# Optimization experiments

Measured on AMD Instinct MI355X. Metric: run time of the kernel, lower is better.

Reference implementation:

```python
import jax, jax.numpy as jnp
import numpy as np

ALPHA = 1.0
EPS = 1e-8

def setup_inputs() -> dict:
    key = jax.random.key(0)
    k1, k2, k3 = jax.random.split(key, 3)
    B, L, S, H, E, D = 4, 2048, 2048, 8, 64, 64
    queries = jax.random.normal(k1, (B, L, H, E), dtype=jnp.float32)
    keys = jax.random.normal(k2, (B, S, H, E), dtype=jnp.float32)
    values = jax.random.normal(k3, (B, S, H, D), dtype=jnp.float32)
    return {"queries": queries, "keys": keys, "values": values}

def reference(queries, keys, values):
    E = queries.shape[3]
    scale = 1.0 / jnp.sqrt(jnp.asarray(E, queries.dtype))
    # dot_product: [B,H,L,S]
    dot = jnp.einsum('blhe,bshe->bhls', queries, keys)
    q_norm2 = jnp.sum(queries ** 2, axis=-1).transpose(0, 2, 1)[..., :, None]  # [B,H,L,1]
    k_norm2 = jnp.sum(keys ** 2, axis=-1).transpose(0, 2, 1)[..., None, :]     # [B,H,1,S]
    wedge2 = jax.nn.relu(q_norm2 * k_norm2 - dot ** 2)
    wedge = jnp.sqrt(wedge2 + EPS)
    scores = ((1.0 - ALPHA) * dot + ALPHA * wedge) * scale
    A = jax.nn.softmax(scores, axis=-1)  # dropout in eval mode = identity
    out = jnp.einsum('bhls,bshd->blhd', A, values)
    return out
```

## Files before the change

### kernel.cpp

```cpp
#include <hip/hip_runtime.h>

typedef __attribute__((ext_vector_type(4))) float f32x4;
typedef __attribute__((ext_vector_type(4))) float float4v;
typedef __attribute__((ext_vector_type(8))) short bf16x8;
typedef __attribute__((ext_vector_type(8))) unsigned short ushort8;

#define DEVI static __device__ __forceinline__

namespace {
constexpr int kL = 2048, kS = 2048, kH = 8;
constexpr int QB = 64, KVB = 64, NKT = kS / KVB;
constexpr float kC = 0.18033688f;
constexpr float kEpsC = 3.252139e-10f;
constexpr int KTILE = 8448;
constexpr int VTILE = 8192;
constexpr int KBH = 32 * KTILE;
constexpr int VBH = 32 * VTILE;
}

DEVI int swz(int byteoff) { return byteoff ^ (((byteoff >> 7) & 7) << 4); }

DEVI unsigned cvtpk(float lo, float hi) {
  unsigned r;
  asm("v_cvt_pk_bf16_f32 %0, %1, %2" : "=v"(r) : "v"(lo), "v"(hi));
  return r;
}

__global__ __launch_bounds__(256) void prep_k(const float* __restrict__ Kg,
                                              char* __restrict__ Kb) {
  const int chunk = (int)blockIdx.x * 256 + (int)threadIdx.x;
  const int tile = chunk >> 9;
  const int i = chunk & 511;
  const int bh = tile >> 5, kt = tile & 31;
  const int b = bh >> 3, h = bh & 7;
  const int row = i >> 3;
  const int colsel = (i & 7) ^ (row & 7);
  const int s = kt * 64 + row;
  const float* src = Kg + (((size_t)b * kS + s) * kH + h) * 64 + colsel * 8;
  float4v v0 = *(const float4v*)(src);
  float4v v1 = *(const float4v*)(src + 4);
  float pn = v0.x*v0.x + v0.y*v0.y + v0.z*v0.z + v0.w*v0.w
           + v1.x*v1.x + v1.y*v1.y + v1.z*v1.z + v1.w*v1.w;
  union { unsigned w[4]; ushort8 u; } o;
  o.w[0] = cvtpk(v0.x, v0.y); o.w[1] = cvtpk(v0.z, v0.w);
  o.w[2] = cvtpk(v1.x, v1.y); o.w[3] = cvtpk(v1.z, v1.w);
  char* tb = Kb + (size_t)tile * KTILE;
  *(ushort8*)(tb + i * 16) = o.u;
  pn += __shfl_xor(pn, 1);
  pn += __shfl_xor(pn, 2);
  pn += __shfl_xor(pn, 4);
  if ((i & 7) == 0) *(float*)(tb + 8192 + row * 4) = pn;
}

__global__ __launch_bounds__(256) void prep_v(const float* __restrict__ Vg,
                                              char* __restrict__ Vt) {
  __shared__ char tile[64 * 128];
  const int t = (int)threadIdx.x;
  const int bid = (int)blockIdx.x;
  const int st = bid & 31, bh = bid >> 5;
  const int b = bh >> 3, h = bh & 7;
  {
    const int sl = t >> 2, c0 = (t & 3) * 16;
    const float* src = Vg + (((size_t)b * kS + st * 64 + sl) * kH + h) * 64 + c0;
    float4v v0 = *(const float4v*)(src);
    float4v v1 = *(const float4v*)(src + 4);
    float4v v2 = *(const float4v*)(src + 8);
    float4v v3 = *(const float4v*)(src + 12);
    union { unsigned w[4]; ushort8 u; } t0, t1;
    t0.w[0] = cvtpk(v0.x, v0.y); t0.w[1] = cvtpk(v0.z, v0.w);
    t0.w[2] = cvtpk(v1.x, v1.y); t0.w[3] = cvtpk(v1.z, v1.w);
    t1.w[0] = cvtpk(v2.x, v2.y); t1.w[1] = cvtpk(v2.z, v2.w);
    t1.w[2] = cvtpk(v3.x, v3.y); t1.w[3] = cvtpk(v3.z, v3.w);
    *(ushort8*)(tile + swz(sl * 128 + c0 * 2)) = t0.u;
    *(ushort8*)(tile + swz(sl * 128 + c0 * 2 + 16)) = t1.u;
  }
  __syncthreads();
  char* dst = Vt + (size_t)bid * VTILE;
#pragma unroll
  for (int cc = 0; cc < 2; ++cc) {
    const int i = t * 2 + cc;
    const int z = swz(i * 16);
    const int d = z >> 7;
    const int k0 = ((z >> 4) & 7) * 8;
    union { unsigned short s[8]; ushort8 u; } o;
#pragma unroll
    for (int j = 0; j < 8; ++j) {
      const int k = k0 + j;
      const int sig = (((k >> 5) * 2 + ((k & 7) >> 2)) << 4) |
                      (((k >> 3) & 3) << 2) | (k & 3);
      o.s[j] = *(const unsigned short*)(tile + swz(sig * 128 + d * 2));
    }
    *(ushort8*)(dst + i * 16) = o.u;
  }
}

__global__ __launch_bounds__(256) void geo_attn_kernel(
    const float* __restrict__ Qg, const char* __restrict__ Kb,
    const char* __restrict__ Vt, float* __restrict__ Og) {
  __shared__ char lds[2][16384];

  const int t = (int)threadIdx.x;
  const int wv = t >> 6, lane = t & 63, gg = lane >> 4, cl = lane & 15;
  const int bh = (int)blockIdx.y, b = bh >> 3, h = bh & 7;
  const int l0 = (int)blockIdx.x * QB;

  const int q = l0 + wv * 16 + cl;
  const float* qp = Qg + (((size_t)b * kL + q) * kH + h) * 64;
  float4v x0 = *(const float4v*)(qp + gg * 8);
  float4v x1 = *(const float4v*)(qp + gg * 8 + 4);
  float4v x2 = *(const float4v*)(qp + gg * 8 + 32);
  float4v x3 = *(const float4v*)(qp + gg * 8 + 36);
  x0 *= kC; x1 *= kC; x2 *= kC; x3 *= kC;
  float pn = 0.f;
#pragma unroll
  for (int j = 0; j < 4; ++j) {
    pn = fmaf(x0[j], x0[j], pn); pn = fmaf(x1[j], x1[j], pn);
    pn = fmaf(x2[j], x2[j], pn); pn = fmaf(x3[j], x3[j], pn);
  }
  union frag { bf16x8 v; unsigned w[4]; };
  frag qb0, qb1;
  qb0.w[0] = cvtpk(x0.x, x0.y); qb0.w[1] = cvtpk(x0.z, x0.w);
  qb0.w[2] = cvtpk(x1.x, x1.y); qb0.w[3] = cvtpk(x1.z, x1.w);
  qb1.w[0] = cvtpk(x2.x, x2.y); qb1.w[1] = cvtpk(x2.z, x2.w);
  qb1.w[2] = cvtpk(x3.x, x3.y); qb1.w[3] = cvtpk(x3.z, x3.w);
  pn += __shfl_xor(pn, 16);
  pn += __shfl_xor(pn, 32);
  const float qn2 = pn;

  const char* gsrc0 = (wv < 2) ? (Kb + (size_t)bh * KBH) : (Vt + (size_t)bh * VBH);
  const int gstride = (wv < 2) ? KTILE : VTILE;
  const char* gp = gsrc0 + (wv & 1) * 4096 + lane * 16;
  const char* ktail = Kb + (size_t)bh * KBH + 8192;

#define STAGE(BUF) do { \
    char* _lb = lds[BUF] + wv * 4096; \
    __builtin_amdgcn_global_load_lds((__attribute__((address_space(1))) void*)(gp),        (__attribute__((address_space(3))) void*)(_lb),        16, 0, 0); \
    __builtin_amdgcn_global_load_lds((__attribute__((address_space(1))) void*)(gp + 1024), (__attribute__((address_space(3))) void*)(_lb + 1024), 16, 0, 0); \
    __builtin_amdgcn_global_load_lds((__attribute__((address_space(1))) void*)(gp + 2048), (__attribute__((address_space(3))) void*)(_lb + 2048), 16, 0, 0); \
    __builtin_amdgcn_global_load_lds((__attribute__((address_space(1))) void*)(gp + 3072), (__attribute__((address_space(3))) void*)(_lb + 3072), 16, 0, 0); \
  } while (0)

  float lsum = 0.f;
  f32x4 oacc[4];
#pragma unroll
  for (int dt = 0; dt < 4; ++dt) oacc[dt] = (f32x4){0.f, 0.f, 0.f, 0.f};

  STAGE(0);
  gp += gstride;
  __syncthreads();

  int cur = 0;
  for (int kt = 0; kt < NKT; ++kt) {
    if (kt + 1 < NKT) { STAGE(cur ^ 1); gp += gstride; }

    float4v kn2v[4];
#pragma unroll
    for (int nt = 0; nt < 4; ++nt)
      kn2v[nt] = *(const float4v*)(ktail + nt * 64 + gg * 16);
    ktail += KTILE;

    const char* ksc = lds[cur];
    const char* vsc = lds[cur] + 8192;

    f32x4 dacc[4];
#pragma unroll
    for (int nt = 0; nt < 4; ++nt) {
      bf16x8 ka0 = *(const bf16x8*)(ksc + swz((nt * 16 + cl) * 128 + gg * 16));
      bf16x8 ka1 = *(const bf16x8*)(ksc + swz((nt * 16 + cl) * 128 + gg * 16 + 64));
      f32x4 acc = {0.f, 0.f, 0.f, 0.f};
      acc = __builtin_amdgcn_mfma_f32_16x16x32_bf16(ka0, qb0.v, acc, 0, 0, 0);
      acc = __builtin_amdgcn_mfma_f32_16x16x32_bf16(ka1, qb1.v, acc, 0, 0, 0);
      dacc[nt] = acc;
    }

    float sc[4][4];
#pragma unroll
    for (int nt = 0; nt < 4; ++nt)
#pragma unroll
      for (int r = 0; r < 4; ++r) {
        const float dot = dacc[nt][r];
        float w2 = fmaf(-dot, dot, qn2 * kn2v[nt][r]);
        w2 = fmaxf(w2, kEpsC);
        const float p = __builtin_amdgcn_exp2f(__builtin_amdgcn_sqrtf(w2));
        sc[nt][r] = p;
        lsum += p;
      }

    frag pa0, pa1;
    pa0.w[0] = cvtpk(sc[0][0], sc[0][1]); pa0.w[1] = cvtpk(sc[0][2], sc[0][3]);
    pa0.w[2] = cvtpk(sc[1][0], sc[1][1]); pa0.w[3] = cvtpk(sc[1][2], sc[1][3]);
    pa1.w[0] = cvtpk(sc[2][0], sc[2][1]); pa1.w[1] = cvtpk(sc[2][2], sc[2][3]);
    pa1.w[2] = cvtpk(sc[3][0], sc[3][1]); pa1.w[3] = cvtpk(sc[3][2], sc[3][3]);

#pragma unroll
    for (int dt = 0; dt < 4; ++dt) {
      bf16x8 vb0 = *(const bf16x8*)(vsc + swz((dt * 16 + cl) * 128 + gg * 16));
      bf16x8 vb1 = *(const bf16x8*)(vsc + swz((dt * 16 + cl) * 128 + gg * 16 + 64));
      f32x4 acc = oacc[dt];
      acc = __builtin_amdgcn_mfma_f32_16x16x32_bf16(pa0.v, vb0, acc, 0, 0, 0);
      acc = __builtin_amdgcn_mfma_f32_16x16x32_bf16(pa1.v, vb1, acc, 0, 0, 0);
      oacc[dt] = acc;
    }

    __syncthreads();
    cur ^= 1;
  }
#undef STAGE

  lsum += __shfl_xor(lsum, 16);
  lsum += __shfl_xor(lsum, 32);
  const float inv = 1.f / lsum;
  float inv4[4];
#pragma unroll
  for (int r = 0; r < 4; ++r)
    inv4[r] = __shfl(inv, (lane & 48) | (gg * 4 + r));
#pragma unroll
  for (int r = 0; r < 4; ++r) {
    const int l = l0 + wv * 16 + gg * 4 + r;
    float* op = Og + (((size_t)b * kL + l) * kH + h) * 64;
#pragma unroll
    for (int dt = 0; dt < 4; ++dt)
      op[dt * 16 + cl] = oacc[dt][r] * inv4[r];
  }
}

extern "C" void kernel_launch(void* const* d_in, const int* in_sizes, int n_in,
                              void* d_out, int out_size, void* d_ws, size_t ws_size,
                              hipStream_t stream) {
  const float* Qg = (const float*)d_in[0];
  const float* Kg = (const float*)d_in[1];
  const float* Vg = (const float*)d_in[2];
  float* Og = (float*)d_out;
  char* Kb = (char*)d_ws;
  char* Vt = (char*)d_ws + (size_t)1024 * KTILE;
  prep_k<<<2048, 256, 0, stream>>>(Kg, Kb);
  prep_v<<<1024, 256, 0, stream>>>(Vg, Vt);
  dim3 grid(kL / QB, 32);
  geo_attn_kernel<<<grid, dim3(256), 0, stream>>>(Qg, Kb, Vt, Og);
}
```

Measured before the change: 83.96 us.

## Software-pipeline PV MFMA one tile behind QK with triple-buffered V

Restructures the KV loop so the P·V MFMAs for the previous tile run right after the current tile's Q·K MFMAs, before the transcendental score math. The aim is to overlap matrix-core work with the sqrt/exp2 VALU work. K stays double-buffered while V gets a third LDS buffer so the previous tile's V remains valid. This raises LDS use from 32KB to 40KB per block, which may lower occupancy, and adds an epilogue that drains the last pending PV step.

Result: no change. 84.57 us (+0.7%).

```diff
diff --git a/kernel.cpp b/kernel.cpp
--- a/kernel.cpp
+++ b/kernel.cpp
@@ -97,7 +97,8 @@
 __global__ __launch_bounds__(256) void geo_attn_kernel(
     const float* __restrict__ Qg, const char* __restrict__ Kb,
     const char* __restrict__ Vt, float* __restrict__ Og) {
-  __shared__ char lds[2][16384];
+  __shared__ char kbuf[2][8192];
+  __shared__ char vbuf[3][8192];
 
   const int t = (int)threadIdx.x;
   const int wv = t >> 6, lane = t & 63, gg = lane >> 4, cl = lane & 15;
@@ -127,13 +128,14 @@
   pn += __shfl_xor(pn, 32);
   const float qn2 = pn;
 
-  const char* gsrc0 = (wv < 2) ? (Kb + (size_t)bh * KBH) : (Vt + (size_t)bh * VBH);
-  const int gstride = (wv < 2) ? KTILE : VTILE;
-  const char* gp = gsrc0 + (wv & 1) * 4096 + lane * 16;
+  const bool isK = (wv < 2);
+  const char* gp = (isK ? Kb + (size_t)bh * KBH : Vt + (size_t)bh * VBH)
+                   + (wv & 1) * 4096 + lane * 16;
+  const int gstride = isK ? KTILE : VTILE;
   const char* ktail = Kb + (size_t)bh * KBH + 8192;
 
-#define STAGE(BUF) do { \
-    char* _lb = lds[BUF] + wv * 4096; \
+#define STAGE(DSTBASE) do { \
+    char* _lb = (DSTBASE) + (wv & 1) * 4096; \
     __builtin_amdgcn_global_load_lds((__attribute__((address_space(1))) void*)(gp),        (__attribute__((address_space(3))) void*)(_lb),        16, 0, 0); \
     __builtin_amdgcn_global_load_lds((__attribute__((address_space(1))) void*)(gp + 1024), (__attribute__((address_space(3))) void*)(_lb + 1024), 16, 0, 0); \
     __builtin_amdgcn_global_load_lds((__attribute__((address_space(1))) void*)(gp + 2048), (__attribute__((address_space(3))) void*)(_lb + 2048), 16, 0, 0); \
@@ -145,67 +147,89 @@
 #pragma unroll
   for (int dt = 0; dt < 4; ++dt) oacc[dt] = (f32x4){0.f, 0.f, 0.f, 0.f};
 
-  STAGE(0);
+  STAGE(isK ? kbuf[0] : vbuf[0]);
   gp += gstride;
   __syncthreads();
 
-  int cur = 0;
+  char* kr = kbuf[0]; char* kst = kbuf[1];
+  char* vr = vbuf[2]; char* vm = vbuf[0]; char* vst = vbuf[1];
+  frag pa0, pa1;
+  pa0.w[0] = pa0.w[1] = pa0.w[2] = pa0.w[3] = 0u;
+  pa1.w[0] = pa1.w[1] = pa1.w[2] = pa1.w[3] = 0u;
+
   for (int kt = 0; kt < NKT; ++kt) {
-    if (kt + 1 < NKT) { STAGE(cur ^ 1); gp += gstride; }
+    if (kt + 1 < NKT) {
+      STAGE(isK ? kst : vst);
+      gp += gstride;
+    }
 
     float4v kn2v[4];
 #pragma unroll
     for (int nt = 0; nt < 4; ++nt)
       kn2v[nt] = *(const float4v*)(ktail + nt * 64 + gg * 16);
     ktail += KTILE;
-
-    const char* ksc = lds[cur];
-    const char* vsc = lds[cur] + 8192;
+    float qk2[4][4];
+#pragma unroll
+    for (int nt = 0; nt < 4; ++nt)
+#pragma unroll
+      for (int r = 0; r < 4; ++r) qk2[nt][r] = qn2 * kn2v[nt][r];
 
     f32x4 dacc[4];
 #pragma unroll
     for (int nt = 0; nt < 4; ++nt) {
-      bf16x8 ka0 = *(const bf16x8*)(ksc + swz((nt * 16 + cl) * 128 + gg * 16));
-      bf16x8 ka1 = *(const bf16x8*)(ksc + swz((nt * 16 + cl) * 128 + gg * 16 + 64));
+      bf16x8 ka0 = *(const bf16x8*)(kr + swz((nt * 16 + cl) * 128 + gg * 16));
+      bf16x8 ka1 = *(const bf16x8*)(kr + swz((nt * 16 + cl) * 128 + gg * 16 + 64));
       f32x4 acc = {0.f, 0.f, 0.f, 0.f};
       acc = __builtin_amdgcn_mfma_f32_16x16x32_bf16(ka0, qb0.v, acc, 0, 0, 0);
       acc = __builtin_amdgcn_mfma_f32_16x16x32_bf16(ka1, qb1.v, acc, 0, 0, 0);
       dacc[nt] = acc;
     }
 
+    if (kt > 0) {
+#pragma unroll
+      for (int dt = 0; dt < 4; ++dt) {
+        bf16x8 vb0 = *(const bf16x8*)(vr + swz((dt * 16 + cl) * 128 + gg * 16));
+        bf16x8 vb1 = *(const bf16x8*)(vr + swz((dt * 16 + cl) * 128 + gg * 16 + 64));
+        f32x4 acc = oacc[dt];
+        acc = __builtin_amdgcn_mfma_f32_16x16x32_bf16(pa0.v, vb0, acc, 0, 0, 0);
+        acc = __builtin_amdgcn_mfma_f32_16x16x32_bf16(pa1.v, vb1, acc, 0, 0, 0);
+        oacc[dt] = acc;
+      }
+    }
+
     float sc[4][4];
 #pragma unroll
     for (int nt = 0; nt < 4; ++nt)
 #pragma unroll
       for (int r = 0; r < 4; ++r) {
         const float dot = dacc[nt][r];
-        float w2 = fmaf(-dot, dot, qn2 * kn2v[nt][r]);
+        float w2 = fmaf(-dot, dot, qk2[nt][r]);
         w2 = fmaxf(w2, kEpsC);
         const float p = __builtin_amdgcn_exp2f(__builtin_amdgcn_sqrtf(w2));
         sc[nt][r] = p;
         lsum += p;
       }
 
-    frag pa0, pa1;
     pa0.w[0] = cvtpk(sc[0][0], sc[0][1]); pa0.w[1] = cvtpk(sc[0][2], sc[0][3]);
     pa0.w[2] = cvtpk(sc[1][0], sc[1][1]); pa0.w[3] = cvtpk(sc[1][2], sc[1][3]);
     pa1.w[0] = cvtpk(sc[2][0], sc[2][1]); pa1.w[1] = cvtpk(sc[2][2], sc[2][3]);
     pa1.w[2] = cvtpk(sc[3][0], sc[3][1]); pa1.w[3] = cvtpk(sc[3][2], sc[3][3]);
 
-#pragma unroll
-    for (int dt = 0; dt < 4; ++dt) {
-      bf16x8 vb0 = *(const bf16x8*)(vsc + swz((dt * 16 + cl) * 128 + gg * 16));
-      bf16x8 vb1 = *(const bf16x8*)(vsc + swz((dt * 16 + cl) * 128 + gg * 16 + 64));
-      f32x4 acc = oacc[dt];
-      acc = __builtin_amdgcn_mfma_f32_16x16x32_bf16(pa0.v, vb0, acc, 0, 0, 0);
-      acc = __builtin_amdgcn_mfma_f32_16x16x32_bf16(pa1.v, vb1, acc, 0, 0, 0);
-      oacc[dt] = acc;
-    }
-
     __syncthreads();
-    cur ^= 1;
+    { char* tmp = kr; kr = kst; kst = tmp; }
+    { char* tmp = vr; vr = vm; vm = vst; vst = tmp; }
   }
 #undef STAGE
+
+#pragma unroll
+  for (int dt = 0; dt < 4; ++dt) {
+    bf16x8 vb0 = *(const bf16x8*)(vr + swz((dt * 16 + cl) * 128 + gg * 16));
+    bf16x8 vb1 = *(const bf16x8*)(vr + swz((dt * 16 + cl) * 128 + gg * 16 + 64));
+    f32x4 acc = oacc[dt];
+    acc = __builtin_amdgcn_mfma_f32_16x16x32_bf16(pa0.v, vb0, acc, 0, 0, 0);
+    acc = __builtin_amdgcn_mfma_f32_16x16x32_bf16(pa1.v, vb1, acc, 0, 0, 0);
+    oacc[dt] = acc;
+  }
 
   lsum += __shfl_xor(lsum, 16);
   lsum += __shfl_xor(lsum, 32);
```

## Compute softmax row sums via MFMA, pack score math, remap blocks, prefetch k-norms

Applied to the files above, without the earlier changes.

Replaces the per-lane scalar accumulation of exp scores with an MFMA against a ones vector, so the row sum comes out in the output layout and the final cross-lane shuffles go away. The wedge computation uses packed two-wide float math and fabs in place of the max-with-epsilon clamp. The k-norm loads are software-pipelined one tile ahead, and the grid is flattened with a swizzled block-to-(bh, l) mapping, which changes which blocks share K/V data in cache. Launch bounds now request 4 blocks per CU. The row sum is taken over the bf16-rounded probabilities, which changes numerics slightly, and dropping the epsilon changes results for near-zero wedge values.

Result: faster. 74.66 us (-11.1%).

```diff
diff --git a/kernel.cpp b/kernel.cpp
--- a/kernel.cpp
+++ b/kernel.cpp
@@ -1,5 +1,6 @@
 #include <hip/hip_runtime.h>
 
+typedef __attribute__((ext_vector_type(2))) float f32x2;
 typedef __attribute__((ext_vector_type(4))) float f32x4;
 typedef __attribute__((ext_vector_type(4))) float float4v;
 typedef __attribute__((ext_vector_type(8))) short bf16x8;
@@ -11,7 +12,6 @@
 constexpr int kL = 2048, kS = 2048, kH = 8;
 constexpr int QB = 64, KVB = 64, NKT = kS / KVB;
 constexpr float kC = 0.18033688f;
-constexpr float kEpsC = 3.252139e-10f;
 constexpr int KTILE = 8448;
 constexpr int VTILE = 8192;
 constexpr int KBH = 32 * KTILE;
@@ -94,15 +94,17 @@
   }
 }
 
-__global__ __launch_bounds__(256) void geo_attn_kernel(
+__global__ __launch_bounds__(256, 4) void geo_attn_kernel(
     const float* __restrict__ Qg, const char* __restrict__ Kb,
     const char* __restrict__ Vt, float* __restrict__ Og) {
   __shared__ char lds[2][16384];
 
   const int t = (int)threadIdx.x;
   const int wv = t >> 6, lane = t & 63, gg = lane >> 4, cl = lane & 15;
-  const int bh = (int)blockIdx.y, b = bh >> 3, h = bh & 7;
-  const int l0 = (int)blockIdx.x * QB;
+  const int n = (int)blockIdx.x;
+  const int bh = (n & 7) * 4 + ((n >> 3) & 3);
+  const int l0 = (n >> 5) * QB;
+  const int b = bh >> 3, h = bh & 7;
 
   const int q = l0 + wv * 16 + cl;
   const float* qp = Qg + (((size_t)b * kL + q) * kH + h) * 64;
@@ -125,11 +127,15 @@
   qb1.w[2] = cvtpk(x3.x, x3.y); qb1.w[3] = cvtpk(x3.z, x3.w);
   pn += __shfl_xor(pn, 16);
   pn += __shfl_xor(pn, 32);
-  const float qn2 = pn;
-
-  const char* gsrc0 = (wv < 2) ? (Kb + (size_t)bh * KBH) : (Vt + (size_t)bh * VBH);
-  const int gstride = (wv < 2) ? KTILE : VTILE;
-  const char* gp = gsrc0 + (wv & 1) * 4096 + lane * 16;
+  const f32x2 qn2p = {pn, pn};
+
+  frag vone;
+  vone.w[0] = vone.w[1] = vone.w[2] = vone.w[3] = 0x3F803F80u;
+
+  const bool isK = (wv < 2);
+  const char* gp = (isK ? Kb + (size_t)bh * KBH : Vt + (size_t)bh * VBH)
+                   + (wv & 1) * 4096 + lane * 16;
+  const int gstride = isK ? KTILE : VTILE;
   const char* ktail = Kb + (size_t)bh * KBH + 8192;
 
 #define STAGE(BUF) do { \
@@ -140,23 +146,28 @@
     __builtin_amdgcn_global_load_lds((__attribute__((address_space(1))) void*)(gp + 3072), (__attribute__((address_space(3))) void*)(_lb + 3072), 16, 0, 0); \
   } while (0)
 
-  float lsum = 0.f;
   f32x4 oacc[4];
 #pragma unroll
   for (int dt = 0; dt < 4; ++dt) oacc[dt] = (f32x4){0.f, 0.f, 0.f, 0.f};
+  f32x4 lacc = (f32x4){0.f, 0.f, 0.f, 0.f};
 
   STAGE(0);
   gp += gstride;
+  float4v kn2r[4];
+#pragma unroll
+  for (int nt = 0; nt < 4; ++nt)
+    kn2r[nt] = *(const float4v*)(ktail + nt * 64 + gg * 16);
+  ktail += KTILE;
   __syncthreads();
 
   int cur = 0;
   for (int kt = 0; kt < NKT; ++kt) {
     if (kt + 1 < NKT) { STAGE(cur ^ 1); gp += gstride; }
 
-    float4v kn2v[4];
+    float4v kn2n[4];
 #pragma unroll
     for (int nt = 0; nt < 4; ++nt)
-      kn2v[nt] = *(const float4v*)(ktail + nt * 64 + gg * 16);
+      kn2n[nt] = *(const float4v*)(ktail + nt * 64 + gg * 16);
     ktail += KTILE;
 
     const char* ksc = lds[cur];
@@ -173,24 +184,20 @@
       dacc[nt] = acc;
     }
 
-    float sc[4][4];
-#pragma unroll
-    for (int nt = 0; nt < 4; ++nt)
-#pragma unroll
-      for (int r = 0; r < 4; ++r) {
-        const float dot = dacc[nt][r];
-        float w2 = fmaf(-dot, dot, qn2 * kn2v[nt][r]);
-        w2 = fmaxf(w2, kEpsC);
-        const float p = __builtin_amdgcn_exp2f(__builtin_amdgcn_sqrtf(w2));
-        sc[nt][r] = p;
-        lsum += p;
-      }
-
+    unsigned pw[8];
+#pragma unroll
+    for (int i = 0; i < 8; ++i) {
+      const int nt = i >> 1, hh = (i & 1) * 2;
+      const f32x2 d2 = {dacc[nt][hh], dacc[nt][hh + 1]};
+      const f32x2 k2 = {kn2r[nt][hh], kn2r[nt][hh + 1]};
+      const f32x2 w2 = qn2p * k2 - d2 * d2;
+      const float p0 = __builtin_amdgcn_exp2f(__builtin_amdgcn_sqrtf(fabsf(w2.x)));
+      const float p1 = __builtin_amdgcn_exp2f(__builtin_amdgcn_sqrtf(fabsf(w2.y)));
+      pw[i] = cvtpk(p0, p1);
+    }
     frag pa0, pa1;
-    pa0.w[0] = cvtpk(sc[0][0], sc[0][1]); pa0.w[1] = cvtpk(sc[0][2], sc[0][3]);
-    pa0.w[2] = cvtpk(sc[1][0], sc[1][1]); pa0.w[3] = cvtpk(sc[1][2], sc[1][3]);
-    pa1.w[0] = cvtpk(sc[2][0], sc[2][1]); pa1.w[1] = cvtpk(sc[2][2], sc[2][3]);
-    pa1.w[2] = cvtpk(sc[3][0], sc[3][1]); pa1.w[3] = cvtpk(sc[3][2], sc[3][3]);
+    pa0.w[0] = pw[0]; pa0.w[1] = pw[1]; pa0.w[2] = pw[2]; pa0.w[3] = pw[3];
+    pa1.w[0] = pw[4]; pa1.w[1] = pw[5]; pa1.w[2] = pw[6]; pa1.w[3] = pw[7];
 
 #pragma unroll
     for (int dt = 0; dt < 4; ++dt) {
@@ -201,26 +208,25 @@
       acc = __builtin_amdgcn_mfma_f32_16x16x32_bf16(pa1.v, vb1, acc, 0, 0, 0);
       oacc[dt] = acc;
     }
+    lacc = __builtin_amdgcn_mfma_f32_16x16x32_bf16(pa0.v, vone.v, lacc, 0, 0, 0);
+    lacc = __builtin_amdgcn_mfma_f32_16x16x32_bf16(pa1.v, vone.v, lacc, 0, 0, 0);
+
+#pragma unroll
+    for (int nt = 0; nt < 4; ++nt) kn2r[nt] = kn2n[nt];
 
     __syncthreads();
     cur ^= 1;
   }
 #undef STAGE
 
-  lsum += __shfl_xor(lsum, 16);
-  lsum += __shfl_xor(lsum, 32);
-  const float inv = 1.f / lsum;
-  float inv4[4];
-#pragma unroll
-  for (int r = 0; r < 4; ++r)
-    inv4[r] = __shfl(inv, (lane & 48) | (gg * 4 + r));
 #pragma unroll
   for (int r = 0; r < 4; ++r) {
     const int l = l0 + wv * 16 + gg * 4 + r;
+    const float inv = 1.f / lacc[r];
     float* op = Og + (((size_t)b * kL + l) * kH + h) * 64;
 #pragma unroll
     for (int dt = 0; dt < 4; ++dt)
-      op[dt * 16 + cl] = oacc[dt][r] * inv4[r];
+      op[dt * 16 + cl] = oacc[dt][r] * inv;
   }
 }
 
@@ -235,6 +241,5 @@
   char* Vt = (char*)d_ws + (size_t)1024 * KTILE;
   prep_k<<<2048, 256, 0, stream>>>(Kg, Kb);
   prep_v<<<1024, 256, 0, stream>>>(Vg, Vt);
-  dim3 grid(kL / QB, 32);
-  geo_attn_kernel<<<grid, dim3(256), 0, stream>>>(Qg, Kb, Vt, Og);
-}
+  geo_attn_kernel<<<dim3(1024), dim3(256), 0, stream>>>(Qg, Kb, Vt, Og);
+}
```
